# Performance work log

Measured on AMD Instinct MI355X. Metric: run time of the kernel, lower is better.

Reference implementation:

```python
import jax, jax.numpy as jnp
import numpy as np

HIDDEN = 2048
N_HEADS = 16
HEAD_DIM = HIDDEN // N_HEADS
SEQ = 4096
ROPE_BASE = 10000.0


def setup_inputs() -> dict:
    key = jax.random.key(0)
    ks = jax.random.split(key, 5)
    sc = 1.0 / np.sqrt(HIDDEN)
    return {
        "hidden_states": jax.random.normal(ks[0], (SEQ, HIDDEN), jnp.float32),
        "Wq": jax.random.normal(ks[1], (HIDDEN, HIDDEN), jnp.float32) * sc,
        "Wk": jax.random.normal(ks[2], (HIDDEN, HIDDEN), jnp.float32) * sc,
        "Wv": jax.random.normal(ks[3], (HIDDEN, HIDDEN), jnp.float32) * sc,
        "Wo": jax.random.normal(ks[4], (HIDDEN, HIDDEN), jnp.float32) * sc,
    }


def _rope_cos_sin(seq_len, head_dim, dtype):
    # Llama-style rotary embedding tables, shape [S, 1, head_dim]
    inv_freq = 1.0 / (ROPE_BASE ** (jnp.arange(0, head_dim, 2, dtype=jnp.float32) / head_dim))
    pos = jnp.arange(seq_len, dtype=jnp.float32)
    freqs = pos[:, None] * inv_freq[None, :]          # [S, d/2]
    emb = jnp.concatenate([freqs, freqs], axis=-1)     # [S, d]
    return jnp.cos(emb)[:, None, :].astype(dtype), jnp.sin(emb)[:, None, :].astype(dtype)


def _rotate_half(x):
    h = x.shape[-1] // 2
    return jnp.concatenate([-x[..., h:], x[..., :h]], axis=-1)


def reference(hidden_states, Wq, Wk, Wv, Wo):
    S, H = hidden_states.shape
    d = HEAD_DIM
    # QKV projections (nn.Linear: x @ W.T), split into heads: [S, nH, d]
    q = (hidden_states @ Wq.T).reshape(S, N_HEADS, d)
    k = (hidden_states @ Wk.T).reshape(S, N_HEADS, d)
    v = (hidden_states @ Wv.T).reshape(S, N_HEADS, d)
    # Per-position RoPE on q and k
    cos, sin = _rope_cos_sin(S, d, q.dtype)
    q = q * cos + _rotate_half(q) * sin
    k = k * cos + _rotate_half(k) * sin
    # Causal scaled-dot-product attention, scores [nH, S, S]
    scores = jnp.einsum("snd,tnd->nst", q, k) / jnp.sqrt(jnp.asarray(d, q.dtype))
    causal = jnp.tril(jnp.ones((S, S), dtype=bool))
    scores = jnp.where(causal[None, :, :], scores, jnp.asarray(-1e30, scores.dtype))
    probs = jax.nn.softmax(scores, axis=-1)
    ctx = jnp.einsum("nst,tnd->snd", probs, v).reshape(S, H)
    return ctx @ Wo.T
```

## Files before the change

### kernel.cpp

```cpp
#include <hip/hip_runtime.h>

#define SEQ 4096
#define HIDDEN 2048
#define NHEADS 16
#define HDIM 128
#define QBLK 128
#define KVB 64

typedef float f32x4 __attribute__((ext_vector_type(4)));
typedef __bf16 bf16x8 __attribute__((ext_vector_type(8)));
typedef unsigned int u32x4 __attribute__((ext_vector_type(4)));
typedef unsigned short u16x8 __attribute__((ext_vector_type(8)));
typedef unsigned short u16;

#define SCL2 0.12751747456918851f
#define RLOG 0.2076205059304601f

__device__ __forceinline__ u16 f2bf(float f) {
  unsigned u = __float_as_uint(f);
  unsigned r = 0x7fffu + ((u >> 16) & 1u);
  return (u16)((u + r) >> 16);
}
__device__ __forceinline__ float bf2f(u16 u) {
  return __uint_as_float(((unsigned)u) << 16);
}
__device__ __forceinline__ unsigned cvtpk(float a, float b) {
  unsigned r;
  asm volatile("v_cvt_pk_bf16_f32 %0, %1, %2" : "=v"(r) : "v"(a), "v"(b));
  return r;
}

__device__ __forceinline__ void gload16(const u16* g, u16* l) {
  __builtin_amdgcn_global_load_lds(
      (const __attribute__((address_space(1))) unsigned int*)g,
      (__attribute__((address_space(3))) unsigned int*)l, 16, 0, 0);
}

__device__ __forceinline__ int cumq(int q) {
  return q < 24 ? (q - 12) * 2 : 24 + (q - 24) * 3;
}

__global__ __launch_bounds__(256) void cvt5(const float* __restrict__ X,
    const float* __restrict__ Wq, const float* __restrict__ Wk,
    const float* __restrict__ Wv, const float* __restrict__ Wo,
    u16* __restrict__ dst) {
  const size_t SH = (size_t)SEQ * HIDDEN, HH = (size_t)HIDDEN * HIDDEN;
  size_t i = ((size_t)blockIdx.x * 256 + threadIdx.x) * 8;
  const float* src; size_t off;
  if (i < SH) { src = X; off = i; }
  else if (i < SH + HH) { src = Wq; off = i - SH; }
  else if (i < SH + 2 * HH) { src = Wk; off = i - SH - HH; }
  else if (i < SH + 3 * HH) { src = Wv; off = i - SH - 2 * HH; }
  else { src = Wo; off = i - SH - 3 * HH; }
  float4 a = *reinterpret_cast<const float4*>(src + off);
  float4 b = *reinterpret_cast<const float4*>(src + off + 4);
  u16x8 o;
  o[0] = f2bf(a.x); o[1] = f2bf(a.y); o[2] = f2bf(a.z); o[3] = f2bf(a.w);
  o[4] = f2bf(b.x); o[5] = f2bf(b.y); o[6] = f2bf(b.z); o[7] = f2bf(b.w);
  *reinterpret_cast<u32x4*>(dst + i) = __builtin_bit_cast(u32x4, o);
}

__global__ __launch_bounds__(256, 3) void gemm_qkv(const u16* __restrict__ Xb,
    const u16* __restrict__ Wqb, const u16* __restrict__ Wkb,
    const u16* __restrict__ Wvb, u16* __restrict__ Qo, u16* __restrict__ Ko,
    u16* __restrict__ Vt) {
  __shared__ u16 As[3][4096];
  __shared__ u16 Bs[3][4096];
  const int wg = blockIdx.x;
  const int swz = (wg & 7) * 192 + (wg >> 3);
  const int z = swz >> 9;
  const int rr_ = swz & 511;
  const u16 *A, *B;
  u16* C;
  int bm, bn, cst;
  if (z == 2) {
    A = Wvb; B = Xb; C = Vt;
    bm = (rr_ & 15) << 7; bn = (rr_ >> 4) << 7; cst = SEQ;
  } else {
    A = Xb; B = z ? Wkb : Wqb; C = z ? Ko : Qo;
    bm = (rr_ & 31) << 7; bn = (rr_ >> 5) << 7; cst = HIDDEN;
  }
  const int t = threadIdx.x, lane = t & 63, wave = t >> 6;
  const int lrow = lane & 15, lgrp = lane >> 4;
  const int wr = wave * 32;
  const int r0 = t >> 2;
  const int c0 = ((t & 3) ^ ((r0 >> 1) & 3)) * 8;
  const int ksx8 = (lgrp ^ ((lrow >> 1) & 3)) * 8;

  f32x4 acc[2][8] = {};

  const u16* Ab = A + (size_t)(bm + r0) * HIDDEN + c0;
  const u16* Bb = B + (size_t)(bn + r0) * HIDDEN + c0;
  const size_t rstep = (size_t)64 * HIDDEN;

#define QKV_STAGE(tt, s)                                            \
  {                                                                 \
    const int ko = (tt) * 32;                                       \
    gload16(Ab + ko, &As[s][t * 8]);                                \
    gload16(Bb + ko, &Bs[s][t * 8]);                                \
    gload16(Ab + rstep + ko, &As[s][2048 + t * 8]);                 \
    gload16(Bb + rstep + ko, &Bs[s][2048 + t * 8]);                 \
  }

  QKV_STAGE(0, 0);
  QKV_STAGE(1, 1);
  asm volatile("s_waitcnt vmcnt(4)" ::: "memory");
  __builtin_amdgcn_s_barrier();
  asm volatile("" ::: "memory");

  int sa = 0, sb = 1, sc = 2;
  for (int tt = 0; tt < 64; ++tt) {
    if (tt + 2 < 64) QKV_STAGE(tt + 2, sc);
    bf16x8 af[2], bfv[8];
#pragma unroll
    for (int m = 0; m < 2; ++m)
      af[m] = __builtin_bit_cast(bf16x8,
          *reinterpret_cast<const u32x4*>(&As[sa][(wr + m * 16 + lrow) * 32 + ksx8]));
#pragma unroll
    for (int n = 0; n < 8; ++n)
      bfv[n] = __builtin_bit_cast(bf16x8,
          *reinterpret_cast<const u32x4*>(&Bs[sa][(n * 16 + lrow) * 32 + ksx8]));
#pragma unroll
    for (int n = 0; n < 8; ++n)
#pragma unroll
      for (int m = 0; m < 2; ++m)
        acc[m][n] = __builtin_amdgcn_mfma_f32_16x16x32_bf16(af[m], bfv[n], acc[m][n], 0, 0, 0);
    asm volatile("s_waitcnt vmcnt(4)" ::: "memory");
    __builtin_amdgcn_sched_barrier(0);
    __builtin_amdgcn_s_barrier();
    asm volatile("" ::: "memory");
    int s_ = sa; sa = sb; sb = sc; sc = s_;
  }
#undef QKV_STAGE

  const int rb = (lane >> 4) * 4;
  if (z < 2) {
    const float qscale = (z == 0) ? SCL2 : 1.0f;
#pragma unroll
    for (int m = 0; m < 2; ++m)
#pragma unroll
      for (int q = 0; q < 4; ++q) {
        const int s = bm + wr + m * 16 + rb + q;
#pragma unroll
        for (int n = 0; n < 4; ++n) {
          const int ii = n * 16 + lrow;
          float inv = exp2f((float)ii * -RLOG);
          float ang = (float)s * inv;
          float sn, cs;
          __sincosf(ang, &sn, &cs);
          sn *= qscale; cs *= qscale;
          float x1 = acc[m][n][q], x2 = acc[m][n + 4][q];
          acc[m][n][q] = x1 * cs - x2 * sn;
          acc[m][n + 4][q] = x2 * cs + x1 * sn;
        }
      }
  }
#pragma unroll
  for (int m = 0; m < 2; ++m)
#pragma unroll
    for (int n = 0; n < 8; ++n)
#pragma unroll
      for (int q = 0; q < 4; ++q) {
        int col;
        if (z == 2)
          col = bn + (n >> 2) * 64 + ((n >> 1) & 1) * 32 + (lrow >> 2) * 8 +
                (n & 1) * 4 + (lrow & 3);
        else
          col = bn + n * 16 + lrow;
        C[(size_t)(bm + wr + m * 16 + rb + q) * cst + col] = f2bf(acc[m][n][q]);
      }
}

__global__ __launch_bounds__(256, 3) void gemm_out(const u16* __restrict__ A,
    const u16* __restrict__ B, float* __restrict__ C) {
  __shared__ u16 As[3][4096];
  __shared__ u16 Bs[3][4096];
  const int wg = blockIdx.x;
  const int swz = (wg & 7) * 64 + (wg >> 3);
  const int bm = (swz & 31) << 7;
  const int bn = (swz >> 5) << 7;
  const int t = threadIdx.x, lane = t & 63, wave = t >> 6;
  const int lrow = lane & 15, lgrp = lane >> 4;
  const int wr = wave * 32;
  const int r0 = t >> 2;
  const int c0 = ((t & 3) ^ ((r0 >> 1) & 3)) * 8;
  const int ksx8 = (lgrp ^ ((lrow >> 1) & 3)) * 8;

  f32x4 acc[2][8] = {};

  const u16* Ab = A + (size_t)(bm + r0) * HIDDEN + c0;
  const u16* Bb = B + (size_t)(bn + r0) * HIDDEN + c0;
  const size_t rstep = (size_t)64 * HIDDEN;

#define OUT_STAGE(tt, s)                                            \
  {                                                                 \
    const int ko = (tt) * 32;                                       \
    gload16(Ab + ko, &As[s][t * 8]);                                \
    gload16(Bb + ko, &Bs[s][t * 8]);                                \
    gload16(Ab + rstep + ko, &As[s][2048 + t * 8]);                 \
    gload16(Bb + rstep + ko, &Bs[s][2048 + t * 8]);                 \
  }

  OUT_STAGE(0, 0);
  OUT_STAGE(1, 1);
  asm volatile("s_waitcnt vmcnt(4)" ::: "memory");
  __builtin_amdgcn_s_barrier();
  asm volatile("" ::: "memory");

  int sa = 0, sb = 1, sc = 2;
  for (int tt = 0; tt < 64; ++tt) {
    if (tt + 2 < 64) OUT_STAGE(tt + 2, sc);
    bf16x8 af[2], bfv[8];
#pragma unroll
    for (int m = 0; m < 2; ++m)
      af[m] = __builtin_bit_cast(bf16x8,
          *reinterpret_cast<const u32x4*>(&As[sa][(wr + m * 16 + lrow) * 32 + ksx8]));
#pragma unroll
    for (int n = 0; n < 8; ++n)
      bfv[n] = __builtin_bit_cast(bf16x8,
          *reinterpret_cast<const u32x4*>(&Bs[sa][(n * 16 + lrow) * 32 + ksx8]));
#pragma unroll
    for (int n = 0; n < 8; ++n)
#pragma unroll
      for (int m = 0; m < 2; ++m)
        acc[m][n] = __builtin_amdgcn_mfma_f32_16x16x32_bf16(af[m], bfv[n], acc[m][n], 0, 0, 0);
    asm volatile("s_waitcnt vmcnt(4)" ::: "memory");
    __builtin_amdgcn_sched_barrier(0);
    __builtin_amdgcn_s_barrier();
    asm volatile("" ::: "memory");
    int s_ = sa; sa = sb; sb = sc; sc = s_;
  }
#undef OUT_STAGE

  const int rb = (lane >> 4) * 4;
#pragma unroll
  for (int m = 0; m < 2; ++m)
#pragma unroll
    for (int n = 0; n < 8; ++n)
#pragma unroll
      for (int q = 0; q < 4; ++q)
        C[(size_t)(bm + wr + m * 16 + rb + q) * HIDDEN + bn + n * 16 + lrow] =
            acc[m][n][q];
}

__global__ __launch_bounds__(512, 4) void attn_kernel(const u16* __restrict__ Q,
                                                      const u16* __restrict__ Kg,
                                                      const u16* __restrict__ Vt,
                                                      u16* __restrict__ O,
                                                      u16* __restrict__ Opart,
                                                      float* __restrict__ Ml) {
  __shared__ u16 Ks[2][KVB * 128];
  __shared__ u16 Vs[2][128 * KVB];
  const int t = threadIdx.x;
  const int wave = t >> 6;
  const int lane = t & 63;
  const int lrow = lane & 15;
  const int lgrp = lane >> 4;

  const int g = blockIdx.x;
  const int h = g & 15;
  const int e = g >> 4;
  int q, c, nc;
  if (e < 24)      { q = 24 + e / 3;           c = e % 3;         nc = 3; }
  else if (e < 48) { q = 23 - ((e - 24) >> 1); c = (e - 24) & 1;  nc = 2; }
  else             { q = 59 - e;               c = 0;             nc = 1; }
  const int total = 2 * q + 2;
  const int base = total / nc, rem = total - base * nc;
  const int it0 = c * base + (c < rem ? c : rem);
  const int it1 = it0 + base + (c < rem ? 1 : 0);

  const int qw = q * QBLK + wave * 16;

  bf16x8 qf[4];
#pragma unroll
  for (int kk = 0; kk < 4; ++kk)
    qf[kk] = __builtin_bit_cast(bf16x8, *reinterpret_cast<const u32x4*>(
        Q + (size_t)(qw + lrow) * HIDDEN + h * HDIM + kk * 32 + lgrp * 8));

  u16x8 ow;
#pragma unroll
  for (int j = 0; j < 8; ++j) ow[j] = (lrow == 0) ? 0x3F80 : 0;
  const bf16x8 vones = __builtin_bit_cast(bf16x8, ow);

  const u16* kgb[2]; const u16* vgb[2]; int kof[2], vof[2];
#pragma unroll
  for (int is = 0; is < 2; ++is) {
    int ch = is * 512 + t;
    int krow = ch >> 4, kslot = ch & 15;
    int kcol = ((kslot & 8) | ((kslot ^ krow) & 7)) * 8;
    kgb[is] = Kg + (size_t)krow * HIDDEN + h * HDIM + kcol;
    kof[is] = ch * 8;
    int vrow = ch >> 3, vslot = ch & 7;
    int vcol = ((vslot ^ vrow) & 7) * 8;
    vgb[is] = Vt + (size_t)(h * HDIM + vrow) * SEQ + vcol;
    vof[is] = ch * 8;
  }

  f32x4 acc[8] = {};
  f32x4 acc1 = {};
  float m2 = -1e30f;

#pragma unroll
  for (int is = 0; is < 2; ++is) {
    gload16(kgb[is] + (size_t)(it0 * KVB) * HIDDEN, &Ks[0][kof[is]]);
    gload16(vgb[is] + it0 * KVB, &Vs[0][vof[is]]);
  }
  __syncthreads();

  int p = 0;
  for (int bt = it0; bt < it1; ++bt) {
    const int t0 = bt * KVB;
    if (bt + 1 < it1) {
      const int t1 = (bt + 1) * KVB;
#pragma unroll
      for (int is = 0; is < 2; ++is) {
        gload16(kgb[is] + (size_t)t1 * HIDDEN, &Ks[p ^ 1][kof[is]]);
        gload16(vgb[is] + t1, &Vs[p ^ 1][vof[is]]);
      }
    }

    if (t0 <= qw + 15) {
      const bool need_mask = (t0 + KVB - 1 > qw);
      f32x4 sc[4] = {};
      __builtin_amdgcn_s_setprio(1);
#pragma unroll
      for (int kk = 0; kk < 4; ++kk) {
#pragma unroll
        for (int colf = 0; colf < 4; ++colf) {
          int trow = colf * 16 + lrow;
          int slot = kk * 4 + lgrp;
          bf16x8 kf = __builtin_bit_cast(bf16x8, *reinterpret_cast<const u32x4*>(
              &Ks[p][trow * 128 + ((slot & 8) | ((slot ^ trow) & 7)) * 8]));
          sc[colf] = __builtin_amdgcn_mfma_f32_16x16x32_bf16(kf, qf[kk], sc[colf], 0, 0, 0);
        }
      }
      __builtin_amdgcn_s_setprio(0);

      const int qg = qw + lrow;
      if (need_mask) {
#pragma unroll
        for (int colf = 0; colf < 4; ++colf) {
          const int kvb0 = t0 + colf * 16 + lgrp * 4;
#pragma unroll
          for (int r = 0; r < 4; ++r)
            sc[colf][r] = (kvb0 + r <= qg) ? sc[colf][r] : -1e30f;
        }
      }
      float mc[4];
#pragma unroll
      for (int colf = 0; colf < 4; ++colf)
        mc[colf] = fmaxf(fmaxf(sc[colf][0], sc[colf][1]),
                         fmaxf(sc[colf][2], sc[colf][3]));
      float mx = fmaxf(fmaxf(mc[0], mc[1]), fmaxf(mc[2], mc[3]));
      mx = fmaxf(mx, __shfl_xor(mx, 16));
      mx = fmaxf(mx, __shfl_xor(mx, 32));

      if (__any(mx > m2 + 11.5f)) {
        float mn = fmaxf(m2, mx);
        float sf = exp2f(m2 - mn);
        m2 = mn;
#pragma unroll
        for (int r = 0; r < 4; ++r) {
          float sfr = __shfl(sf, (lane & 48) | (lgrp * 4 + r));
#pragma unroll
          for (int nn = 0; nn < 8; ++nn) acc[nn][r] *= sfr;
          acc1[r] *= sfr;
        }
      }

      unsigned paw[2][4];
#pragma unroll
      for (int colf = 0; colf < 4; ++colf) {
        float pv[4];
#pragma unroll
        for (int r = 0; r < 4; ++r) pv[r] = exp2f(sc[colf][r] - m2);
        paw[colf >> 1][(colf & 1) * 2 + 0] = cvtpk(pv[0], pv[1]);
        paw[colf >> 1][(colf & 1) * 2 + 1] = cvtpk(pv[2], pv[3]);
      }

      __builtin_amdgcn_s_setprio(1);
#pragma unroll
      for (int ks = 0; ks < 2; ++ks) {
        u32x4 w = {paw[ks][0], paw[ks][1], paw[ks][2], paw[ks][3]};
        bf16x8 pa = __builtin_bit_cast(bf16x8, w);
#pragma unroll
        for (int nn = 0; nn < 8; ++nn) {
          const int d = nn * 16 + lrow;
          bf16x8 vb = __builtin_bit_cast(bf16x8, *reinterpret_cast<const u32x4*>(
              &Vs[p][d * 64 + (((ks * 4 + lgrp) ^ d) & 7) * 8]));
          acc[nn] = __builtin_amdgcn_mfma_f32_16x16x32_bf16(pa, vb, acc[nn], 0, 0, 0);
        }
        acc1 = __builtin_amdgcn_mfma_f32_16x16x32_bf16(pa, vones, acc1, 0, 0, 0);
      }
      __builtin_amdgcn_s_setprio(0);
    }

    __syncthreads();
    p ^= 1;
  }

  if (nc == 1) {
    float inv[4];
#pragma unroll
    for (int r = 0; r < 4; ++r)
      inv[r] = 1.0f / __shfl(acc1[r], lane & 48);
#pragma unroll
    for (int nn = 0; nn < 8; ++nn)
#pragma unroll
      for (int r = 0; r < 4; ++r) {
        int row = qw + lgrp * 4 + r;
        int col = h * HDIM + nn * 16 + lrow;
        O[(size_t)row * HIDDEN + col] = f2bf(acc[nn][r] * inv[r]);
      }
  } else {
    const int slot = h * 48 + cumq(q) + c;
    u16* Op = Opart + (size_t)slot * (QBLK * HDIM);
    float* ml = Ml + (size_t)slot * 256;
#pragma unroll
    for (int nn = 0; nn < 8; ++nn)
#pragma unroll
      for (int r = 0; r < 4; ++r) {
        int rl = wave * 16 + lgrp * 4 + r;
        Op[rl * HDIM + nn * 16 + lrow] = f2bf(acc[nn][r]);
      }
    if (lgrp == 0) {
      int rl = wave * 16 + lrow;
      ml[rl] = m2;
    }
    if (lrow == 0) {
#pragma unroll
      for (int r = 0; r < 4; ++r)
        ml[128 + wave * 16 + lgrp * 4 + r] = acc1[r];
    }
  }
}

__global__ __launch_bounds__(256) void combine_kernel(const u16* __restrict__ Opart,
                                                      const float* __restrict__ Ml,
                                                      u16* __restrict__ O) {
  const int bid = blockIdx.x;
  const int h = bid / 20;
  const int q = 12 + bid % 20;
  const int nc = (q < 24) ? 2 : 3;
  const int sbase = h * 48 + cumq(q);
  const int r = threadIdx.x >> 1;
  const int d0 = (threadIdx.x & 1) * 64;

  float w[3], l = 0.f, M = -3.0e38f;
#pragma unroll
  for (int c = 0; c < 3; ++c)
    if (c < nc) M = fmaxf(M, Ml[(size_t)(sbase + c) * 256 + r]);
#pragma unroll
  for (int c = 0; c < 3; ++c)
    if (c < nc) {
      w[c] = exp2f(Ml[(size_t)(sbase + c) * 256 + r] - M);
      l += w[c] * Ml[(size_t)(sbase + c) * 256 + 128 + r];
    }
  const float inv = 1.0f / l;

  for (int dd = 0; dd < 64; dd += 8) {
    float a8[8] = {};
#pragma unroll
    for (int c = 0; c < 3; ++c)
      if (c < nc) {
        u16x8 v = *reinterpret_cast<const u16x8*>(
            Opart + (size_t)(sbase + c) * (QBLK * HDIM) + r * HDIM + d0 + dd);
#pragma unroll
        for (int j = 0; j < 8; ++j) a8[j] += w[c] * bf2f(v[j]);
      }
    u16x8 o8;
#pragma unroll
    for (int j = 0; j < 8; ++j) o8[j] = f2bf(a8[j] * inv);
    *reinterpret_cast<u16x8*>(
        &O[(size_t)(q * QBLK + r) * HIDDEN + h * HDIM + d0 + dd]) = o8;
  }
}

extern "C" void kernel_launch(void* const* d_in, const int* in_sizes, int n_in,
                              void* d_out, int out_size, void* d_ws, size_t ws_size,
                              hipStream_t stream) {
  const float* X  = (const float*)d_in[0];
  const float* Wq = (const float*)d_in[1];
  const float* Wk = (const float*)d_in[2];
  const float* Wv = (const float*)d_in[3];
  const float* Wo = (const float*)d_in[4];
  float* out = (float*)d_out;

  u16* ws = (u16*)d_ws;
  const size_t SH = (size_t)SEQ * HIDDEN;
  const size_t HH = (size_t)HIDDEN * HIDDEN;
  u16* Xb  = ws;
  u16* Wqb = Xb + SH;
  u16* Wkb = Wqb + HH;
  u16* Wvb = Wkb + HH;
  u16* Wob = Wvb + HH;
  u16* Qb  = Wob + HH;
  u16* Kb  = Qb + SH;
  u16* Vtb = Kb + SH;
  u16* Cb  = Vtb + SH;

  u16* Opart = ws;
  float* Ml = (float*)(ws + (size_t)768 * 16384);

  cvt5<<<(int)((SH + 4 * HH) / 2048), 256, 0, stream>>>(X, Wq, Wk, Wv, Wo, ws);

  gemm_qkv<<<1536, 256, 0, stream>>>(Xb, Wqb, Wkb, Wvb, Qb, Kb, Vtb);

  attn_kernel<<<960, 512, 0, stream>>>(Qb, Kb, Vtb, Cb, Opart, Ml);
  combine_kernel<<<320, 256, 0, stream>>>(Opart, Ml, Cb);

  gemm_out<<<512, 256, 0, stream>>>(Cb, Wob, out);
}
```

Before: 328.9 us.

## Switch GEMM wave tiling from 32x128 strips to 2x2 64x64 wave tiles

Changes the per-wave tile in the QKV and output GEMMs from 32 rows by 128 columns to a 2x2 grid of 64x64 tiles. Each wave now reads 4 A and 4 B fragments from LDS per k-step instead of 2 and 8, so LDS reads per MFMA go down. For Q/K, the rows of the B tile are permuted at load time so that the rotate-half pairs (columns i and i+64) land in the same wave, which keeps RoPE fused into the epilogue. The V transposed-store column mapping is rewritten to match the new layout. The change adds index complexity and register pressure.

Result: no change. 323.1 us, median of 3 (-1.7%).

```diff
diff --git a/kernel.cpp b/kernel.cpp
--- a/kernel.cpp
+++ b/kernel.cpp
@@ -82,24 +82,29 @@
   }
   const int t = threadIdx.x, lane = t & 63, wave = t >> 6;
   const int lrow = lane & 15, lgrp = lane >> 4;
-  const int wr = wave * 32;
+  const int wr = (wave >> 1) * 64;
+  const int wc = (wave & 1) * 64;
   const int r0 = t >> 2;
   const int c0 = ((t & 3) ^ ((r0 >> 1) & 3)) * 8;
   const int ksx8 = (lgrp ^ ((lrow >> 1) & 3)) * 8;
 
-  f32x4 acc[2][8] = {};
+  f32x4 acc[4][4] = {};
 
   const u16* Ab = A + (size_t)(bm + r0) * HIDDEN + c0;
-  const u16* Bb = B + (size_t)(bn + r0) * HIDDEN + c0;
-  const size_t rstep = (size_t)64 * HIDDEN;
+  const int nr0 = (z < 2)
+      ? (((r0 >> 4) >> 1) * 16 + (r0 & 15) + ((r0 >> 4) & 1) * 64)
+      : r0;
+  const u16* Bb = B + (size_t)(bn + nr0) * HIDDEN + c0;
+  const size_t rstepA = (size_t)64 * HIDDEN;
+  const size_t rstepB = (size_t)((z < 2) ? 32 : 64) * HIDDEN;
 
 #define QKV_STAGE(tt, s)                                            \
   {                                                                 \
     const int ko = (tt) * 32;                                       \
     gload16(Ab + ko, &As[s][t * 8]);                                \
     gload16(Bb + ko, &Bs[s][t * 8]);                                \
-    gload16(Ab + rstep + ko, &As[s][2048 + t * 8]);                 \
-    gload16(Bb + rstep + ko, &Bs[s][2048 + t * 8]);                 \
+    gload16(Ab + rstepA + ko, &As[s][2048 + t * 8]);                \
+    gload16(Bb + rstepB + ko, &Bs[s][2048 + t * 8]);                \
   }
 
   QKV_STAGE(0, 0);
@@ -111,20 +116,20 @@
   int sa = 0, sb = 1, sc = 2;
   for (int tt = 0; tt < 64; ++tt) {
     if (tt + 2 < 64) QKV_STAGE(tt + 2, sc);
-    bf16x8 af[2], bfv[8];
-#pragma unroll
-    for (int m = 0; m < 2; ++m)
-      af[m] = __builtin_bit_cast(bf16x8,
-          *reinterpret_cast<const u32x4*>(&As[sa][(wr + m * 16 + lrow) * 32 + ksx8]));
-#pragma unroll
-    for (int n = 0; n < 8; ++n)
-      bfv[n] = __builtin_bit_cast(bf16x8,
-          *reinterpret_cast<const u32x4*>(&Bs[sa][(n * 16 + lrow) * 32 + ksx8]));
-#pragma unroll
-    for (int n = 0; n < 8; ++n)
-#pragma unroll
-      for (int m = 0; m < 2; ++m)
-        acc[m][n] = __builtin_amdgcn_mfma_f32_16x16x32_bf16(af[m], bfv[n], acc[m][n], 0, 0, 0);
+    bf16x8 af[4], bfv[4];
+#pragma unroll
+    for (int mf = 0; mf < 4; ++mf)
+      af[mf] = __builtin_bit_cast(bf16x8,
+          *reinterpret_cast<const u32x4*>(&As[sa][(wr + mf * 16 + lrow) * 32 + ksx8]));
+#pragma unroll
+    for (int nf = 0; nf < 4; ++nf)
+      bfv[nf] = __builtin_bit_cast(bf16x8,
+          *reinterpret_cast<const u32x4*>(&Bs[sa][(wc + nf * 16 + lrow) * 32 + ksx8]));
+#pragma unroll
+    for (int nf = 0; nf < 4; ++nf)
+#pragma unroll
+      for (int mf = 0; mf < 4; ++mf)
+        acc[mf][nf] = __builtin_amdgcn_mfma_f32_16x16x32_bf16(af[mf], bfv[nf], acc[mf][nf], 0, 0, 0);
     asm volatile("s_waitcnt vmcnt(4)" ::: "memory");
     __builtin_amdgcn_sched_barrier(0);
     __builtin_amdgcn_s_barrier();
@@ -133,42 +138,41 @@
   }
 #undef QKV_STAGE
 
-  const int rb = (lane >> 4) * 4;
+  const int rb = lgrp * 4;
   if (z < 2) {
     const float qscale = (z == 0) ? SCL2 : 1.0f;
 #pragma unroll
-    for (int m = 0; m < 2; ++m)
-#pragma unroll
-      for (int q = 0; q < 4; ++q) {
-        const int s = bm + wr + m * 16 + rb + q;
-#pragma unroll
-        for (int n = 0; n < 4; ++n) {
-          const int ii = n * 16 + lrow;
-          float inv = exp2f((float)ii * -RLOG);
+    for (int mf = 0; mf < 4; ++mf)
+#pragma unroll
+      for (int j = 0; j < 2; ++j) {
+        const int ii = (((wc >> 4) + 2 * j) >> 1) * 16 + lrow;
+        const float inv = exp2f((float)ii * -RLOG);
+#pragma unroll
+        for (int qq = 0; qq < 4; ++qq) {
+          const int s = bm + wr + mf * 16 + rb + qq;
           float ang = (float)s * inv;
           float sn, cs;
           __sincosf(ang, &sn, &cs);
           sn *= qscale; cs *= qscale;
-          float x1 = acc[m][n][q], x2 = acc[m][n + 4][q];
-          acc[m][n][q] = x1 * cs - x2 * sn;
-          acc[m][n + 4][q] = x2 * cs + x1 * sn;
+          float x1 = acc[mf][2 * j][qq], x2 = acc[mf][2 * j + 1][qq];
+          C[(size_t)s * cst + bn + ii] = f2bf(x1 * cs - x2 * sn);
+          C[(size_t)s * cst + bn + ii + 64] = f2bf(x2 * cs + x1 * sn);
         }
       }
-  }
-#pragma unroll
-  for (int m = 0; m < 2; ++m)
-#pragma unroll
-    for (int n = 0; n < 8; ++n)
-#pragma unroll
-      for (int q = 0; q < 4; ++q) {
-        int col;
-        if (z == 2)
-          col = bn + (n >> 2) * 64 + ((n >> 1) & 1) * 32 + (lrow >> 2) * 8 +
-                (n & 1) * 4 + (lrow & 3);
-        else
-          col = bn + n * 16 + lrow;
-        C[(size_t)(bm + wr + m * 16 + rb + q) * cst + col] = f2bf(acc[m][n][q]);
-      }
+  } else {
+#pragma unroll
+    for (int mf = 0; mf < 4; ++mf)
+#pragma unroll
+      for (int nf = 0; nf < 4; ++nf) {
+        const int col = bn + wc + ((nf >> 1) & 1) * 32 + (lrow >> 2) * 8 +
+                        (nf & 1) * 4 + (lrow & 3);
+#pragma unroll
+        for (int qq = 0; qq < 4; ++qq) {
+          const int s = bm + wr + mf * 16 + rb + qq;
+          C[(size_t)s * cst + col] = f2bf(acc[mf][nf][qq]);
+        }
+      }
+  }
 }
 
 __global__ __launch_bounds__(256, 3) void gemm_out(const u16* __restrict__ A,
@@ -181,12 +185,13 @@
   const int bn = (swz >> 5) << 7;
   const int t = threadIdx.x, lane = t & 63, wave = t >> 6;
   const int lrow = lane & 15, lgrp = lane >> 4;
-  const int wr = wave * 32;
+  const int wr = (wave >> 1) * 64;
+  const int wc = (wave & 1) * 64;
   const int r0 = t >> 2;
   const int c0 = ((t & 3) ^ ((r0 >> 1) & 3)) * 8;
   const int ksx8 = (lgrp ^ ((lrow >> 1) & 3)) * 8;
 
-  f32x4 acc[2][8] = {};
+  f32x4 acc[4][4] = {};
 
   const u16* Ab = A + (size_t)(bm + r0) * HIDDEN + c0;
   const u16* Bb = B + (size_t)(bn + r0) * HIDDEN + c0;
@@ -210,20 +215,20 @@
   int sa = 0, sb = 1, sc = 2;
   for (int tt = 0; tt < 64; ++tt) {
     if (tt + 2 < 64) OUT_STAGE(tt + 2, sc);
-    bf16x8 af[2], bfv[8];
-#pragma unroll
-    for (int m = 0; m < 2; ++m)
-      af[m] = __builtin_bit_cast(bf16x8,
-          *reinterpret_cast<const u32x4*>(&As[sa][(wr + m * 16 + lrow) * 32 + ksx8]));
-#pragma unroll
-    for (int n = 0; n < 8; ++n)
-      bfv[n] = __builtin_bit_cast(bf16x8,
-          *reinterpret_cast<const u32x4*>(&Bs[sa][(n * 16 + lrow) * 32 + ksx8]));
-#pragma unroll
-    for (int n = 0; n < 8; ++n)
-#pragma unroll
-      for (int m = 0; m < 2; ++m)
-        acc[m][n] = __builtin_amdgcn_mfma_f32_16x16x32_bf16(af[m], bfv[n], acc[m][n], 0, 0, 0);
+    bf16x8 af[4], bfv[4];
+#pragma unroll
+    for (int mf = 0; mf < 4; ++mf)
+      af[mf] = __builtin_bit_cast(bf16x8,
+          *reinterpret_cast<const u32x4*>(&As[sa][(wr + mf * 16 + lrow) * 32 + ksx8]));
+#pragma unroll
+    for (int nf = 0; nf < 4; ++nf)
+      bfv[nf] = __builtin_bit_cast(bf16x8,
+          *reinterpret_cast<const u32x4*>(&Bs[sa][(wc + nf * 16 + lrow) * 32 + ksx8]));
+#pragma unroll
+    for (int nf = 0; nf < 4; ++nf)
+#pragma unroll
+      for (int mf = 0; mf < 4; ++mf)
+        acc[mf][nf] = __builtin_amdgcn_mfma_f32_16x16x32_bf16(af[mf], bfv[nf], acc[mf][nf], 0, 0, 0);
     asm volatile("s_waitcnt vmcnt(4)" ::: "memory");
     __builtin_amdgcn_sched_barrier(0);
     __builtin_amdgcn_s_barrier();
@@ -232,15 +237,15 @@
   }
 #undef OUT_STAGE
 
-  const int rb = (lane >> 4) * 4;
-#pragma unroll
-  for (int m = 0; m < 2; ++m)
-#pragma unroll
-    for (int n = 0; n < 8; ++n)
-#pragma unroll
-      for (int q = 0; q < 4; ++q)
-        C[(size_t)(bm + wr + m * 16 + rb + q) * HIDDEN + bn + n * 16 + lrow] =
-            acc[m][n][q];
+  const int rb = lgrp * 4;
+#pragma unroll
+  for (int mf = 0; mf < 4; ++mf)
+#pragma unroll
+    for (int nf = 0; nf < 4; ++nf)
+#pragma unroll
+      for (int qq = 0; qq < 4; ++qq)
+        C[(size_t)(bm + wr + mf * 16 + rb + qq) * HIDDEN + bn + wc + nf * 16 + lrow] =
+            acc[mf][nf][qq];
 }
 
 __global__ __launch_bounds__(512, 4) void attn_kernel(const u16* __restrict__ Q,
```
